# Kernel optimization log

Hardware: AMD Instinct MI355X
Metric: run time of the kernel (lower is better)

## Reference

```python
import jax, jax.numpy as jnp
import numpy as np

N = 50000
D_IN = 512
D_OUT = 512
NUM_SAMPLE = 2


def setup_inputs() -> dict:
    key = jax.random.key(0)
    ks = jax.random.split(key, 8)
    x = jax.random.normal(ks[0], (N, D_IN), dtype=jnp.float32)
    neighs1 = jax.random.randint(ks[1], (N, NUM_SAMPLE), 0, N, dtype=jnp.int32)
    neighs2 = jax.random.randint(ks[2], (N, NUM_SAMPLE), 0, N, dtype=jnp.int32)
    # SageLayer weights: [out, 2*in] (self || aggregated neighbors), xavier-ish scale
    W1 = jax.random.normal(ks[3], (D_OUT, 2 * D_IN), dtype=jnp.float32) * 0.03
    W2 = jax.random.normal(ks[4], (D_OUT, 2 * D_OUT), dtype=jnp.float32) * 0.03
    fc_w = jax.random.normal(ks[5], (2, N * D_OUT), dtype=jnp.float32) * 0.0005
    fc_b = jnp.zeros((2,), dtype=jnp.float32)
    return {"x": x, "neighs1": neighs1, "neighs2": neighs2,
            "W1": W1, "W2": W2, "fc_w": fc_w, "fc_b": fc_b}


def _sage_layer(h, neighs, W):
    # MEAN aggregation over the num_sample sampled neighbors (self excluded, gcn=False).
    # Equivalent to the original dense one-hot mask.div(num_neigh).mm(embed_matrix).
    agg = h[neighs].mean(axis=1)                      # [N, S, d] -> [N, d]
    combined = jnp.concatenate([h, agg], axis=1)      # [N, 2d]
    # F.relu(W.mm(combined.t())).t() == relu(combined @ W.T)
    return jax.nn.relu(combined @ W.T)                # [N, out]


def reference(x, neighs1, neighs2, W1, W2, fc_w, fc_b):
    h = _sage_layer(x, neighs1, W1)
    h = _sage_layer(h, neighs2, W2)
    flat = h.reshape(1, -1)                           # [1, N*out]
    logits = flat @ fc_w.T + fc_b                     # [1, 2]
    return (flat, jax.nn.log_softmax(logits, axis=1))
```

## Files before the change

kernel.cpp:

```cpp
#include <hip/hip_runtime.h>
#include <stdint.h>

typedef short bf16x8 __attribute__((ext_vector_type(8)));
typedef float f32x4 __attribute__((ext_vector_type(4)));
typedef unsigned short u16x8 __attribute__((ext_vector_type(8)));

#define N_NODES 50000
#define DIM 512
#define TDIM 1024
#define NPAD 50048
#define M_TILES 391
#define GEMM_GRID 3136
#define FLAT_TOTAL 25600000ULL
#define NBLK_COMB 12500

__device__ __forceinline__ unsigned short f2bf(float f) {
    unsigned u = __float_as_uint(f);
    unsigned r = u + 0x7FFFu + ((u >> 16) & 1u);
    return (unsigned short)(r >> 16);
}
__device__ __forceinline__ float bf2f(unsigned short h) {
    return __uint_as_float(((unsigned)h) << 16);
}

__device__ __forceinline__ void llds16(const void* g, void* l) {
    __builtin_amdgcn_global_load_lds(
        (const __attribute__((address_space(1))) void*)g,
        (__attribute__((address_space(3))) void*)l,
        16, 0, 0);
}

__global__ void cast_x(const float* __restrict__ x, unsigned short* __restrict__ o) {
    size_t i = ((size_t)blockIdx.x * blockDim.x + threadIdx.x) * 8;
    float4 v0 = *(const float4*)&x[i];
    float4 v1 = *(const float4*)&x[i + 4];
    u16x8 r;
    r[0] = f2bf(v0.x); r[1] = f2bf(v0.y); r[2] = f2bf(v0.z); r[3] = f2bf(v0.w);
    r[4] = f2bf(v1.x); r[5] = f2bf(v1.y); r[6] = f2bf(v1.z); r[7] = f2bf(v1.w);
    *(u16x8*)&o[i] = r;
}

__global__ void cast_w_split2(const float* __restrict__ w1, const float* __restrict__ w2,
                              unsigned short* __restrict__ o1, unsigned short* __restrict__ o2) {
    int b = blockIdx.x;
    const float* w = (b < 256) ? w1 : w2;
    unsigned short* o = (b < 256) ? o1 : o2;
    int idx = ((b & 255) * 256 + threadIdx.x) * 8;
    int j = idx >> 9;
    int k = idx & 511;
    size_t src = (j < 512) ? ((size_t)j * 1024 + k) : ((size_t)(j - 512) * 1024 + 512 + k);
    float4 v0 = *(const float4*)&w[src];
    float4 v1 = *(const float4*)&w[src + 4];
    u16x8 r;
    r[0] = f2bf(v0.x); r[1] = f2bf(v0.y); r[2] = f2bf(v0.z); r[3] = f2bf(v0.w);
    r[4] = f2bf(v1.x); r[5] = f2bf(v1.y); r[6] = f2bf(v1.z); r[7] = f2bf(v1.w);
    *(u16x8*)&o[idx] = r;
}

__global__ __launch_bounds__(256)
void gemm_nt(const unsigned short* __restrict__ A, const unsigned short* __restrict__ B,
             unsigned short* __restrict__ T) {
    __shared__ unsigned short As[2][128 * 32];
    __shared__ unsigned short Bs[2][128 * 32];

    int x = blockIdx.x & 7;
    int g = blockIdx.x >> 3;
    int bm = x + 8 * (g >> 3);
    int bn = g & 7;
    if (bm >= M_TILES) return;

    int t = threadIdx.x;
    int lane = t & 63;
    int wave = t >> 6;
    int m_off = (wave >> 1) * 64;
    int n_off = (wave & 1) * 64;
    int lrow = lane & 15;
    int lk = (lane >> 4) * 8;

    f32x4 acc[4][4];
#pragma unroll
    for (int i = 0; i < 4; i++)
#pragma unroll
        for (int j = 0; j < 4; j++) acc[i][j] = (f32x4){0.f, 0.f, 0.f, 0.f};

    const unsigned short* ga = A + (size_t)(bm * 128 + (t >> 2)) * DIM + (t & 3) * 8;
    const unsigned short* gb = B + (size_t)(bn * 128 + (t >> 2)) * DIM + (t & 3) * 8;

    for (int k0 = 0; k0 < DIM; k0 += 64) {
        __syncthreads();
        llds16(ga + k0,            &As[0][t * 8]);
        llds16(ga + k0 + 64 * DIM, &As[0][t * 8 + 2048]);
        llds16(gb + k0,            &Bs[0][t * 8]);
        llds16(gb + k0 + 64 * DIM, &Bs[0][t * 8 + 2048]);
        llds16(ga + k0 + 32,            &As[1][t * 8]);
        llds16(ga + k0 + 32 + 64 * DIM, &As[1][t * 8 + 2048]);
        llds16(gb + k0 + 32,            &Bs[1][t * 8]);
        llds16(gb + k0 + 32 + 64 * DIM, &Bs[1][t * 8 + 2048]);
        __syncthreads();

#pragma unroll
        for (int h = 0; h < 2; h++) {
            bf16x8 af[4], bfr[4];
#pragma unroll
            for (int i = 0; i < 4; i++)
                af[i] = *(const bf16x8*)&As[h][(m_off + i * 16 + lrow) * 32 + lk];
#pragma unroll
            for (int j = 0; j < 4; j++)
                bfr[j] = *(const bf16x8*)&Bs[h][(n_off + j * 16 + lrow) * 32 + lk];
#pragma unroll
            for (int i = 0; i < 4; i++)
#pragma unroll
                for (int j = 0; j < 4; j++)
                    acc[i][j] = __builtin_amdgcn_mfma_f32_16x16x32_bf16(af[i], bfr[j], acc[i][j], 0, 0, 0);
        }
    }

    int lc = lane & 15;
    int lr = (lane >> 4) << 2;
#pragma unroll
    for (int i = 0; i < 4; i++) {
        int row0 = bm * 128 + m_off + i * 16 + lr;
#pragma unroll
        for (int j = 0; j < 4; j++) {
            int col = bn * 128 + n_off + j * 16 + lc;
            f32x4 v = acc[i][j];
#pragma unroll
            for (int r = 0; r < 4; r++)
                T[(size_t)(row0 + r) * TDIM + col] = f2bf(v[r]);
        }
    }
}

__global__ void combine1(const unsigned short* __restrict__ T, const int* __restrict__ nb,
                         unsigned short* __restrict__ H) {
    int t = threadIdx.x;
    int i = blockIdx.x * 4 + (t >> 6);
    int lane = t & 63;
    int c = lane * 8;
    int n0 = nb[i * 2], n1 = nb[i * 2 + 1];
    u16x8 p  = *(const u16x8*)&T[(size_t)i  * TDIM + c];
    u16x8 q0 = *(const u16x8*)&T[(size_t)n0 * TDIM + 512 + c];
    u16x8 q1 = *(const u16x8*)&T[(size_t)n1 * TDIM + 512 + c];
    u16x8 o;
#pragma unroll
    for (int j = 0; j < 8; j++)
        o[j] = f2bf(fmaxf(bf2f(p[j]) + 0.5f * (bf2f(q0[j]) + bf2f(q1[j])), 0.f));
    *(u16x8*)&H[(size_t)i * DIM + c] = o;
}

__global__ void combine2(const unsigned short* __restrict__ T, const int* __restrict__ nb,
                         const float* __restrict__ fcw, float* __restrict__ out,
                         float2* __restrict__ partials) {
    int t = threadIdx.x;
    int i = blockIdx.x * 4 + (t >> 6);
    int lane = t & 63;
    int w = t >> 6;
    int c = lane * 8;
    int n0 = nb[i * 2], n1 = nb[i * 2 + 1];
    u16x8 p  = *(const u16x8*)&T[(size_t)i  * TDIM + c];
    u16x8 q0 = *(const u16x8*)&T[(size_t)n0 * TDIM + 512 + c];
    u16x8 q1 = *(const u16x8*)&T[(size_t)n1 * TDIM + 512 + c];
    float v[8];
#pragma unroll
    for (int j = 0; j < 8; j++)
        v[j] = fmaxf(bf2f(p[j]) + 0.5f * (bf2f(q0[j]) + bf2f(q1[j])), 0.f);
    size_t ob = (size_t)i * DIM + c;
    *(float4*)&out[ob]     = (float4){v[0], v[1], v[2], v[3]};
    *(float4*)&out[ob + 4] = (float4){v[4], v[5], v[6], v[7]};
    float4 a0 = *(const float4*)&fcw[ob];
    float4 a1 = *(const float4*)&fcw[ob + 4];
    float4 b0 = *(const float4*)&fcw[FLAT_TOTAL + ob];
    float4 b1 = *(const float4*)&fcw[FLAT_TOTAL + ob + 4];
    float s0 = v[0]*a0.x + v[1]*a0.y + v[2]*a0.z + v[3]*a0.w
             + v[4]*a1.x + v[5]*a1.y + v[6]*a1.z + v[7]*a1.w;
    float s1 = v[0]*b0.x + v[1]*b0.y + v[2]*b0.z + v[3]*b0.w
             + v[4]*b1.x + v[5]*b1.y + v[6]*b1.z + v[7]*b1.w;
#pragma unroll
    for (int off = 32; off > 0; off >>= 1) {
        s0 += __shfl_down(s0, off);
        s1 += __shfl_down(s1, off);
    }
    __shared__ float r0[4], r1[4];
    if (lane == 0) { r0[w] = s0; r1[w] = s1; }
    __syncthreads();
    if (t == 0)
        partials[blockIdx.x] = make_float2(r0[0] + r0[1] + r0[2] + r0[3],
                                           r1[0] + r1[1] + r1[2] + r1[3]);
}

__global__ void reduce_finalize(const float2* __restrict__ partials, const float* __restrict__ fcb,
                                float* __restrict__ out2) {
    float s0 = 0.f, s1 = 0.f;
    for (int k = threadIdx.x; k < NBLK_COMB; k += 1024) {
        float2 pr = partials[k];
        s0 += pr.x; s1 += pr.y;
    }
#pragma unroll
    for (int off = 32; off > 0; off >>= 1) {
        s0 += __shfl_down(s0, off);
        s1 += __shfl_down(s1, off);
    }
    __shared__ float r0[16], r1[16];
    int lane = threadIdx.x & 63, w = threadIdx.x >> 6;
    if (lane == 0) { r0[w] = s0; r1[w] = s1; }
    __syncthreads();
    if (threadIdx.x == 0) {
        float l0 = fcb[0], l1 = fcb[1];
#pragma unroll
        for (int k = 0; k < 16; k++) { l0 += r0[k]; l1 += r1[k]; }
        float m = fmaxf(l0, l1);
        float lse = m + logf(expf(l0 - m) + expf(l1 - m));
        out2[0] = l0 - lse;
        out2[1] = l1 - lse;
    }
}

extern "C" void kernel_launch(void* const* d_in, const int* in_sizes, int n_in,
                              void* d_out, int out_size, void* d_ws, size_t ws_size,
                              hipStream_t stream) {
    const float* x   = (const float*)d_in[0];
    const int*   n1  = (const int*)d_in[1];
    const int*   n2  = (const int*)d_in[2];
    const float* W1  = (const float*)d_in[3];
    const float* W2  = (const float*)d_in[4];
    const float* fcw = (const float*)d_in[5];
    const float* fcb = (const float*)d_in[6];
    float* out = (float*)d_out;

    char* ws = (char*)d_ws;
    const size_t XB_OFF  = 0;
    const size_t T_OFF   = XB_OFF + (size_t)NPAD * DIM * 2;
    const size_t H1_OFF  = T_OFF + (size_t)NPAD * TDIM * 2;
    const size_t W1_OFF  = H1_OFF + (size_t)NPAD * DIM * 2;
    const size_t W2_OFF  = W1_OFF + (size_t)TDIM * DIM * 2;
    const size_t P_OFF   = W2_OFF + (size_t)TDIM * DIM * 2;
    unsigned short* Xb  = (unsigned short*)(ws + XB_OFF);
    unsigned short* T   = (unsigned short*)(ws + T_OFF);
    unsigned short* H1  = (unsigned short*)(ws + H1_OFF);
    unsigned short* W1s = (unsigned short*)(ws + W1_OFF);
    unsigned short* W2s = (unsigned short*)(ws + W2_OFF);
    float2* partials    = (float2*)(ws + P_OFF);

    cast_w_split2<<<512, 256, 0, stream>>>(W1, W2, W1s, W2s);
    cast_x<<<12500, 256, 0, stream>>>(x, Xb);

    gemm_nt<<<GEMM_GRID, 256, 0, stream>>>(Xb, W1s, T);
    combine1<<<NBLK_COMB, 256, 0, stream>>>(T, n1, H1);
    gemm_nt<<<GEMM_GRID, 256, 0, stream>>>(H1, W2s, T);
    combine2<<<NBLK_COMB, 256, 0, stream>>>(T, n2, fcw, out, partials);

    reduce_finalize<<<1, 1024, 0, stream>>>(partials, fcb, out + FLAT_TOTAL);
}
```

Before: 551.6 us.

## Aggregate neighbors before the GEMM and fuse ReLU into the GEMM epilogue

Reorders each SAGE layer to average the neighbor features first and then run one GEMM with K=1024 over the self and aggregated inputs. ReLU moves into the GEMM epilogue, and the second layer writes fp32 output directly. This replaces the wide N×1024 intermediate and its combine kernels with narrower N×512 gather buffers. In exchange, the FC dot product now needs a separate pass that re-reads the flat output, and the aggregates are rounded to bf16 before the matmul.

```diff
diff --git a/kernel.cpp b/kernel.cpp
--- a/kernel.cpp
+++ b/kernel.cpp
@@ -7,12 +7,12 @@
 
 #define N_NODES 50000
 #define DIM 512
-#define TDIM 1024
+#define KDIM 1024
 #define NPAD 50048
 #define M_TILES 391
-#define GEMM_GRID 3136
+#define GEMM_GRID 1568
 #define FLAT_TOTAL 25600000ULL
-#define NBLK_COMB 12500
+#define NBLK_FC 2048
 
 __device__ __forceinline__ unsigned short f2bf(float f) {
     unsigned u = __float_as_uint(f);
@@ -40,33 +40,46 @@
     *(u16x8*)&o[i] = r;
 }
 
-__global__ void cast_w_split2(const float* __restrict__ w1, const float* __restrict__ w2,
-                              unsigned short* __restrict__ o1, unsigned short* __restrict__ o2) {
+__global__ void cast_w2(const float* __restrict__ w1, const float* __restrict__ w2,
+                        unsigned short* __restrict__ o1, unsigned short* __restrict__ o2) {
     int b = blockIdx.x;
     const float* w = (b < 256) ? w1 : w2;
     unsigned short* o = (b < 256) ? o1 : o2;
     int idx = ((b & 255) * 256 + threadIdx.x) * 8;
-    int j = idx >> 9;
-    int k = idx & 511;
-    size_t src = (j < 512) ? ((size_t)j * 1024 + k) : ((size_t)(j - 512) * 1024 + 512 + k);
-    float4 v0 = *(const float4*)&w[src];
-    float4 v1 = *(const float4*)&w[src + 4];
+    float4 v0 = *(const float4*)&w[idx];
+    float4 v1 = *(const float4*)&w[idx + 4];
     u16x8 r;
     r[0] = f2bf(v0.x); r[1] = f2bf(v0.y); r[2] = f2bf(v0.z); r[3] = f2bf(v0.w);
     r[4] = f2bf(v1.x); r[5] = f2bf(v1.y); r[6] = f2bf(v1.z); r[7] = f2bf(v1.w);
     *(u16x8*)&o[idx] = r;
 }
 
+__global__ void agg_mean(const unsigned short* __restrict__ H, const int* __restrict__ nb,
+                         unsigned short* __restrict__ G) {
+    int t = threadIdx.x;
+    int i = blockIdx.x * 4 + (t >> 6);
+    int lane = t & 63;
+    int c = lane * 8;
+    int n0 = nb[i * 2], n1 = nb[i * 2 + 1];
+    u16x8 a = *(const u16x8*)&H[(size_t)n0 * DIM + c];
+    u16x8 b = *(const u16x8*)&H[(size_t)n1 * DIM + c];
+    u16x8 o;
+#pragma unroll
+    for (int j = 0; j < 8; j++) o[j] = f2bf((bf2f(a[j]) + bf2f(b[j])) * 0.5f);
+    *(u16x8*)&G[(size_t)i * DIM + c] = o;
+}
+
+template <int OUT_MODE>
 __global__ __launch_bounds__(256)
-void gemm_nt(const unsigned short* __restrict__ A, const unsigned short* __restrict__ B,
-             unsigned short* __restrict__ T) {
+void gemm_fused(const unsigned short* __restrict__ A1, const unsigned short* __restrict__ A2,
+                const unsigned short* __restrict__ B, void* __restrict__ C) {
     __shared__ unsigned short As[2][128 * 32];
     __shared__ unsigned short Bs[2][128 * 32];
 
     int x = blockIdx.x & 7;
     int g = blockIdx.x >> 3;
-    int bm = x + 8 * (g >> 3);
-    int bn = g & 7;
+    int bm = x + 8 * (g >> 2);
+    int bn = g & 3;
     if (bm >= M_TILES) return;
 
     int t = threadIdx.x;
@@ -83,19 +96,21 @@
 #pragma unroll
         for (int j = 0; j < 4; j++) acc[i][j] = (f32x4){0.f, 0.f, 0.f, 0.f};
 
-    const unsigned short* ga = A + (size_t)(bm * 128 + (t >> 2)) * DIM + (t & 3) * 8;
-    const unsigned short* gb = B + (size_t)(bn * 128 + (t >> 2)) * DIM + (t & 3) * 8;
-
-    for (int k0 = 0; k0 < DIM; k0 += 64) {
+    size_t arow = (size_t)(bm * 128 + (t >> 2)) * DIM + (t & 3) * 8;
+    size_t brow = (size_t)(bn * 128 + (t >> 2)) * KDIM + (t & 3) * 8;
+
+    for (int k0 = 0; k0 < KDIM; k0 += 64) {
+        const unsigned short* pa = ((k0 < DIM) ? A1 : A2) + arow + (k0 & (DIM - 1));
+        const unsigned short* pb = B + brow + k0;
         __syncthreads();
-        llds16(ga + k0,            &As[0][t * 8]);
-        llds16(ga + k0 + 64 * DIM, &As[0][t * 8 + 2048]);
-        llds16(gb + k0,            &Bs[0][t * 8]);
-        llds16(gb + k0 + 64 * DIM, &Bs[0][t * 8 + 2048]);
-        llds16(ga + k0 + 32,            &As[1][t * 8]);
-        llds16(ga + k0 + 32 + 64 * DIM, &As[1][t * 8 + 2048]);
-        llds16(gb + k0 + 32,            &Bs[1][t * 8]);
-        llds16(gb + k0 + 32 + 64 * DIM, &Bs[1][t * 8 + 2048]);
+        llds16(pa,                 &As[0][t * 8]);
+        llds16(pa + 64 * DIM,      &As[0][t * 8 + 2048]);
+        llds16(pb,                 &Bs[0][t * 8]);
+        llds16(pb + 64 * KDIM,     &Bs[0][t * 8 + 2048]);
+        llds16(pa + 32,            &As[1][t * 8]);
+        llds16(pa + 32 + 64 * DIM, &As[1][t * 8 + 2048]);
+        llds16(pb + 32,            &Bs[1][t * 8]);
+        llds16(pb + 32 + 64 * KDIM,&Bs[1][t * 8 + 2048]);
         __syncthreads();
 
 #pragma unroll
@@ -124,66 +139,43 @@
         for (int j = 0; j < 4; j++) {
             int col = bn * 128 + n_off + j * 16 + lc;
             f32x4 v = acc[i][j];
-#pragma unroll
-            for (int r = 0; r < 4; r++)
-                T[(size_t)(row0 + r) * TDIM + col] = f2bf(v[r]);
+            if (OUT_MODE == 0) {
+                unsigned short* Cb = (unsigned short*)C;
+#pragma unroll
+                for (int r = 0; r < 4; r++)
+                    Cb[(size_t)(row0 + r) * DIM + col] = f2bf(fmaxf(v[r], 0.f));
+            } else {
+                float* Cf = (float*)C;
+#pragma unroll
+                for (int r = 0; r < 4; r++)
+                    if (row0 + r < N_NODES)
+                        Cf[(size_t)(row0 + r) * DIM + col] = fmaxf(v[r], 0.f);
+            }
         }
     }
 }
 
-__global__ void combine1(const unsigned short* __restrict__ T, const int* __restrict__ nb,
-                         unsigned short* __restrict__ H) {
-    int t = threadIdx.x;
-    int i = blockIdx.x * 4 + (t >> 6);
-    int lane = t & 63;
-    int c = lane * 8;
-    int n0 = nb[i * 2], n1 = nb[i * 2 + 1];
-    u16x8 p  = *(const u16x8*)&T[(size_t)i  * TDIM + c];
-    u16x8 q0 = *(const u16x8*)&T[(size_t)n0 * TDIM + 512 + c];
-    u16x8 q1 = *(const u16x8*)&T[(size_t)n1 * TDIM + 512 + c];
-    u16x8 o;
-#pragma unroll
-    for (int j = 0; j < 8; j++)
-        o[j] = f2bf(fmaxf(bf2f(p[j]) + 0.5f * (bf2f(q0[j]) + bf2f(q1[j])), 0.f));
-    *(u16x8*)&H[(size_t)i * DIM + c] = o;
-}
-
-__global__ void combine2(const unsigned short* __restrict__ T, const int* __restrict__ nb,
-                         const float* __restrict__ fcw, float* __restrict__ out,
-                         float2* __restrict__ partials) {
-    int t = threadIdx.x;
-    int i = blockIdx.x * 4 + (t >> 6);
-    int lane = t & 63;
-    int w = t >> 6;
-    int c = lane * 8;
-    int n0 = nb[i * 2], n1 = nb[i * 2 + 1];
-    u16x8 p  = *(const u16x8*)&T[(size_t)i  * TDIM + c];
-    u16x8 q0 = *(const u16x8*)&T[(size_t)n0 * TDIM + 512 + c];
-    u16x8 q1 = *(const u16x8*)&T[(size_t)n1 * TDIM + 512 + c];
-    float v[8];
-#pragma unroll
-    for (int j = 0; j < 8; j++)
-        v[j] = fmaxf(bf2f(p[j]) + 0.5f * (bf2f(q0[j]) + bf2f(q1[j])), 0.f);
-    size_t ob = (size_t)i * DIM + c;
-    *(float4*)&out[ob]     = (float4){v[0], v[1], v[2], v[3]};
-    *(float4*)&out[ob + 4] = (float4){v[4], v[5], v[6], v[7]};
-    float4 a0 = *(const float4*)&fcw[ob];
-    float4 a1 = *(const float4*)&fcw[ob + 4];
-    float4 b0 = *(const float4*)&fcw[FLAT_TOTAL + ob];
-    float4 b1 = *(const float4*)&fcw[FLAT_TOTAL + ob + 4];
-    float s0 = v[0]*a0.x + v[1]*a0.y + v[2]*a0.z + v[3]*a0.w
-             + v[4]*a1.x + v[5]*a1.y + v[6]*a1.z + v[7]*a1.w;
-    float s1 = v[0]*b0.x + v[1]*b0.y + v[2]*b0.z + v[3]*b0.w
-             + v[4]*b1.x + v[5]*b1.y + v[6]*b1.z + v[7]*b1.w;
+__global__ void fc_reduce(const float* __restrict__ flat, const float* __restrict__ fcw,
+                          float2* __restrict__ partials) {
+    float s0 = 0.f, s1 = 0.f;
+    size_t stride = (size_t)gridDim.x * blockDim.x * 4;
+    for (size_t i = ((size_t)blockIdx.x * blockDim.x + threadIdx.x) * 4; i < FLAT_TOTAL; i += stride) {
+        float4 v  = *(const float4*)&flat[i];
+        float4 w0 = *(const float4*)&fcw[i];
+        float4 w1 = *(const float4*)&fcw[FLAT_TOTAL + i];
+        s0 += v.x * w0.x + v.y * w0.y + v.z * w0.z + v.w * w0.w;
+        s1 += v.x * w1.x + v.y * w1.y + v.z * w1.z + v.w * w1.w;
+    }
 #pragma unroll
     for (int off = 32; off > 0; off >>= 1) {
         s0 += __shfl_down(s0, off);
         s1 += __shfl_down(s1, off);
     }
     __shared__ float r0[4], r1[4];
+    int lane = threadIdx.x & 63, w = threadIdx.x >> 6;
     if (lane == 0) { r0[w] = s0; r1[w] = s1; }
     __syncthreads();
-    if (t == 0)
+    if (threadIdx.x == 0)
         partials[blockIdx.x] = make_float2(r0[0] + r0[1] + r0[2] + r0[3],
                                            r1[0] + r1[1] + r1[2] + r1[3]);
 }
@@ -191,7 +183,7 @@
 __global__ void reduce_finalize(const float2* __restrict__ partials, const float* __restrict__ fcb,
                                 float* __restrict__ out2) {
     float s0 = 0.f, s1 = 0.f;
-    for (int k = threadIdx.x; k < NBLK_COMB; k += 1024) {
+    for (int k = threadIdx.x; k < NBLK_FC; k += 1024) {
         float2 pr = partials[k];
         s0 += pr.x; s1 += pr.y;
     }
@@ -228,26 +220,23 @@
     float* out = (float*)d_out;
 
     char* ws = (char*)d_ws;
-    const size_t XB_OFF  = 0;
-    const size_t T_OFF   = XB_OFF + (size_t)NPAD * DIM * 2;
-    const size_t H1_OFF  = T_OFF + (size_t)NPAD * TDIM * 2;
-    const size_t W1_OFF  = H1_OFF + (size_t)NPAD * DIM * 2;
-    const size_t W2_OFF  = W1_OFF + (size_t)TDIM * DIM * 2;
-    const size_t P_OFF   = W2_OFF + (size_t)TDIM * DIM * 2;
-    unsigned short* Xb  = (unsigned short*)(ws + XB_OFF);
-    unsigned short* T   = (unsigned short*)(ws + T_OFF);
-    unsigned short* H1  = (unsigned short*)(ws + H1_OFF);
-    unsigned short* W1s = (unsigned short*)(ws + W1_OFF);
-    unsigned short* W2s = (unsigned short*)(ws + W2_OFF);
-    float2* partials    = (float2*)(ws + P_OFF);
-
-    cast_w_split2<<<512, 256, 0, stream>>>(W1, W2, W1s, W2s);
+    const size_t HB = (size_t)NPAD * DIM * 2;
+    unsigned short* Xb   = (unsigned short*)(ws);
+    unsigned short* Xag  = (unsigned short*)(ws + HB);
+    unsigned short* H1   = (unsigned short*)(ws + 2 * HB);
+    unsigned short* H1ag = (unsigned short*)(ws + 3 * HB);
+    unsigned short* W1b  = (unsigned short*)(ws + 4 * HB);
+    unsigned short* W2b  = (unsigned short*)(ws + 4 * HB + (size_t)DIM * KDIM * 2);
+    float2* partials     = (float2*)(ws + 4 * HB + 2 * (size_t)DIM * KDIM * 2);
+
+    cast_w2<<<512, 256, 0, stream>>>(W1, W2, W1b, W2b);
     cast_x<<<12500, 256, 0, stream>>>(x, Xb);
 
-    gemm_nt<<<GEMM_GRID, 256, 0, stream>>>(Xb, W1s, T);
-    combine1<<<NBLK_COMB, 256, 0, stream>>>(T, n1, H1);
-    gemm_nt<<<GEMM_GRID, 256, 0, stream>>>(H1, W2s, T);
-    combine2<<<NBLK_COMB, 256, 0, stream>>>(T, n2, fcw, out, partials);
-
+    agg_mean<<<12500, 256, 0, stream>>>(Xb, n1, Xag);
+    gemm_fused<0><<<GEMM_GRID, 256, 0, stream>>>(Xb, Xag, W1b, H1);
+    agg_mean<<<12500, 256, 0, stream>>>(H1, n2, H1ag);
+    gemm_fused<1><<<GEMM_GRID, 256, 0, stream>>>(H1, H1ag, W2b, out);
+
+    fc_reduce<<<NBLK_FC, 256, 0, stream>>>(out, fcw, partials);
     reduce_finalize<<<1, 1024, 0, stream>>>(partials, fcb, out + FLAT_TOTAL);
 }
```

Result: slower. 586.9 us (+6.4%).
